# Performance work log

Hardware: AMD Instinct MI355X
Metric: run time of the kernel (lower is better)

The kernel has to match this reference:

```python
import jax, jax.numpy as jnp
import numpy as np


def _pdists(X):
    # Pairwise Euclidean distances (torch.cdist, p=2) via the Gram trick.
    sq = jnp.sum(X * X, axis=1)                      # (bs,)
    d2 = sq[:, None] + sq[None, :] - 2.0 * (X @ X.T)  # (bs, bs)
    d2 = jnp.maximum(d2, 0.0)
    # safe sqrt: exact forward, finite gradient at 0
    pos = d2 > 0
    return jnp.where(pos, jnp.sqrt(jnp.where(pos, d2, 1.0)), 0.0)


def setup_inputs() -> dict:
    key = jax.random.key(0)
    k1, k2, k3 = jax.random.split(key, 3)
    bs, d = 4096, 512
    n_classes, n_domains = 4, 3
    X = jax.random.normal(k1, (bs, d), dtype=jnp.float32)
    ds = jax.random.randint(k2, (bs,), 0, n_domains, dtype=jnp.int64 if jax.config.read('jax_enable_x64') else jnp.int32)
    y = jax.random.randint(k3, (bs,), 0, n_classes, dtype=jnp.int64 if jax.config.read('jax_enable_x64') else jnp.int32)
    return {"X": X, "ds": ds, "y": y, "n_classes": n_classes, "n_domains": n_domains}


def reference(X, ds, y, n_classes, n_domains):
    # Equivalent to JointCCSA.LSA / JointCCSA.LS with norm=True, assuming every
    # class and domain value appears in the batch (what torch.unique would find).
    dists = _pdists(X)                                # (bs, bs)

    d_lt = ds[:, None] < ds[None, :]                  # domain pair (d1 < d2) ordering
    same_y = y[:, None] == y[None, :]
    y_lt = y[:, None] < y[None, :]                    # class pair (c1 < c2) ordering

    # SA loss: 0.5 * sum over (i,j) with y_i==y_j, ds_i<ds_j
    sa_loss = 0.5 * jnp.sum(jnp.where(same_y & d_lt, dists, 0.0))
    n_sa = n_classes * (n_domains * (n_domains - 1) // 2)
    sa_loss = sa_loss / n_sa

    # S loss: hinge on margin=1, 0.5 * sum over (i,j) with y_i<y_j, ds_i<ds_j
    margin = 1.0
    h = jnp.maximum(0.0, margin - dists)
    s_loss = 0.5 * jnp.sum(jnp.where(y_lt & d_lt, h, 0.0))
    n_s = (n_classes * (n_classes - 1) // 2) * (n_domains * (n_domains - 1) // 2)
    s_loss = s_loss / n_s

    return sa_loss, s_loss
```

## Files before the change

### kernel.cpp

```cpp
#include <hip/hip_runtime.h>
#include <hip/hip_bf16.h>
#include <stdint.h>

#define NROW 4096
#define DIM  512
#define BM   128
#define BN   128
#define BK   64
#define NKT  (DIM / BK)

typedef __attribute__((ext_vector_type(8))) short  short8;
typedef __attribute__((ext_vector_type(4))) float  floatx4;

typedef const __attribute__((address_space(1))) void gvoid_t;
typedef __attribute__((address_space(3))) void       svoid_t;

__device__ __forceinline__ unsigned short f32_to_bf16_rne(float f) {
    unsigned u = __float_as_uint(f);
    u += 0x7FFFu + ((u >> 16) & 1u);
    return (unsigned short)(u >> 16);
}

__global__ __launch_bounds__(256) void prep_kernel(
    const float* __restrict__ X, unsigned short* __restrict__ Xb,
    float* __restrict__ sq, float* __restrict__ out)
{
    const int wave = threadIdx.x >> 6;
    const int lane = threadIdx.x & 63;
    const int row  = blockIdx.x * 4 + wave;
    const float4* xr = (const float4*)(X + (size_t)row * DIM);
    float4 v0 = xr[2 * lane];
    float4 v1 = xr[2 * lane + 1];
    float s = v0.x*v0.x + v0.y*v0.y + v0.z*v0.z + v0.w*v0.w
            + v1.x*v1.x + v1.y*v1.y + v1.z*v1.z + v1.w*v1.w;
    uint4 pk;
    pk.x = f32_to_bf16_rne(v0.x) | ((unsigned)f32_to_bf16_rne(v0.y) << 16);
    pk.y = f32_to_bf16_rne(v0.z) | ((unsigned)f32_to_bf16_rne(v0.w) << 16);
    pk.z = f32_to_bf16_rne(v1.x) | ((unsigned)f32_to_bf16_rne(v1.y) << 16);
    pk.w = f32_to_bf16_rne(v1.z) | ((unsigned)f32_to_bf16_rne(v1.w) << 16);
    *(uint4*)(Xb + (size_t)row * DIM + lane * 8) = pk;
    #pragma unroll
    for (int off = 32; off; off >>= 1) s += __shfl_xor(s, off);
    if (lane == 0) sq[row] = s;
    if (blockIdx.x == 0 && threadIdx.x < 2) out[threadIdx.x] = 0.0f;
}

__global__ __launch_bounds__(256) void ccsa_kernel(
    const unsigned short* __restrict__ Xb, const float* __restrict__ sq,
    const int* __restrict__ ds, const int* __restrict__ y,
    const int* __restrict__ ncls, const int* __restrict__ ndom,
    float* __restrict__ out)
{
    __shared__ __align__(16) unsigned short As[2][BM * BK];
    __shared__ __align__(16) unsigned short Bs[2][BN * BK];
    __shared__ float red[8];

    const int t = blockIdx.x;
    int r = (int)((sqrtf(8.0f * (float)t + 1.0f) - 1.0f) * 0.5f);
    while ((r + 1) * (r + 2) / 2 <= t) ++r;
    while (r * (r + 1) / 2 > t) --r;
    const int bj_t = r;
    const int bi_t = t - r * (r + 1) / 2;
    const bool diag = (bi_t == bj_t);
    const int bm0 = bi_t * BM;
    const int bn0 = bj_t * BN;

    const int tid    = threadIdx.x;
    const int wave   = tid >> 6;
    const int lane   = tid & 63;
    const int warp_m = wave >> 1;
    const int warp_n = wave & 1;

    floatx4 acc[4][4];
    #pragma unroll
    for (int a = 0; a < 4; ++a)
        #pragma unroll
        for (int b = 0; b < 4; ++b)
            acc[a][b] = (floatx4){0.f, 0.f, 0.f, 0.f};

    const int l3       = lane >> 3;
    const int c7       = lane & 7;
    const int srcchunk = c7 ^ l3;
    const int m15      = lane & 15;
    const int quad     = lane >> 4;
    const int row7     = lane & 7;

    #define STAGE(buf, kt)                                                    \
        do {                                                                  \
            const size_t kbase_ = (size_t)(kt) * BK + srcchunk * 8;           \
            _Pragma("unroll")                                                 \
            for (int is = 0; is < 4; ++is) {                                  \
                const int c  = is * 4 + wave;                                 \
                const int rA = bm0 + c * 8 + l3;                              \
                const int rB = bn0 + c * 8 + l3;                              \
                __builtin_amdgcn_global_load_lds(                             \
                    (gvoid_t*)(Xb + (size_t)rA * DIM + kbase_),               \
                    (svoid_t*)(&As[buf][c * 512]), 16, 0, 0);                 \
                __builtin_amdgcn_global_load_lds(                             \
                    (gvoid_t*)(Xb + (size_t)rB * DIM + kbase_),               \
                    (svoid_t*)(&Bs[buf][c * 512]), 16, 0, 0);                 \
            }                                                                 \
        } while (0)

    STAGE(0, 0);
    for (int kt = 0; kt < NKT; ++kt) {
        const int cur = kt & 1;
        __syncthreads();
        if (kt + 1 < NKT) STAGE(cur ^ 1, kt + 1);

        #pragma unroll
        for (int kh = 0; kh < 2; ++kh) {
            short8 a[4], b[4];
            #pragma unroll
            for (int tt = 0; tt < 4; ++tt) {
                const int rla   = warp_m * 64 + tt * 16 + m15;
                const int rlb   = warp_n * 64 + tt * 16 + m15;
                const int chunk = (kh * 4 + quad) ^ row7;
                a[tt] = *(const short8*)(&As[cur][rla * 64 + chunk * 8]);
                b[tt] = *(const short8*)(&Bs[cur][rlb * 64 + chunk * 8]);
            }
            #pragma unroll
            for (int tm = 0; tm < 4; ++tm)
                #pragma unroll
                for (int tn = 0; tn < 4; ++tn)
                    acc[tm][tn] = __builtin_amdgcn_mfma_f32_16x16x32_bf16(
                        a[tm], b[tn], acc[tm][tn], 0, 0, 0);
        }
    }
    #undef STAGE

    float sqj[4]; int yj[4], dsj[4];
    #pragma unroll
    for (int tn = 0; tn < 4; ++tn) {
        const int j = bn0 + warp_n * 64 + tn * 16 + m15;
        sqj[tn] = sq[j]; yj[tn] = y[j]; dsj[tn] = ds[j];
    }
    float sa = 0.f, ss = 0.f;
    if (diag) {
        #pragma unroll
        for (int tm = 0; tm < 4; ++tm) {
            #pragma unroll
            for (int rr = 0; rr < 4; ++rr) {
                const int i = bm0 + warp_m * 64 + tm * 16 + quad * 4 + rr;
                const float sqi = sq[i];
                const int   yi  = y[i];
                const int   dsi = ds[i];
                #pragma unroll
                for (int tn = 0; tn < 4; ++tn) {
                    if (dsi < dsj[tn]) {
                        const float d2   = sqi + sqj[tn] - 2.0f * acc[tm][tn][rr];
                        const float dist = sqrtf(fmaxf(d2, 0.f));
                        if (yi == yj[tn])     sa += dist;
                        else if (yi < yj[tn]) ss += fmaxf(0.f, 1.f - dist);
                    }
                }
            }
        }
    } else {
        #pragma unroll
        for (int tm = 0; tm < 4; ++tm) {
            #pragma unroll
            for (int rr = 0; rr < 4; ++rr) {
                const int i = bm0 + warp_m * 64 + tm * 16 + quad * 4 + rr;
                const float sqi = sq[i];
                const int   yi  = y[i];
                const int   dsi = ds[i];
                #pragma unroll
                for (int tn = 0; tn < 4; ++tn) {
                    if (dsi != dsj[tn]) {
                        const float d2   = sqi + sqj[tn] - 2.0f * acc[tm][tn][rr];
                        const float dist = sqrtf(fmaxf(d2, 0.f));
                        if (yi == yj[tn]) {
                            sa += dist;
                        } else {
                            const bool take = (dsi < dsj[tn]) ? (yi < yj[tn])
                                                              : (yj[tn] < yi);
                            if (take) ss += fmaxf(0.f, 1.f - dist);
                        }
                    }
                }
            }
        }
    }
    #pragma unroll
    for (int off = 32; off; off >>= 1) {
        sa += __shfl_xor(sa, off);
        ss += __shfl_xor(ss, off);
    }
    if (lane == 0) { red[wave] = sa; red[4 + wave] = ss; }
    __syncthreads();
    if (tid == 0) {
        const float tsa = red[0] + red[1] + red[2] + red[3];
        const float tss = red[4] + red[5] + red[6] + red[7];
        const int nc = *ncls, nd = *ndom;
        const float n_sa = (float)(nc * (nd * (nd - 1) / 2));
        const float n_s  = (float)((nc * (nc - 1) / 2) * (nd * (nd - 1) / 2));
        atomicAdd(out + 0, tsa * 0.5f / n_sa);
        atomicAdd(out + 1, tss * 0.5f / n_s);
    }
}

extern "C" void kernel_launch(void* const* d_in, const int* in_sizes, int n_in,
                              void* d_out, int out_size, void* d_ws, size_t ws_size,
                              hipStream_t stream) {
    (void)in_sizes; (void)n_in; (void)out_size; (void)ws_size;
    const float* X  = (const float*)d_in[0];
    const int*   ds = (const int*)d_in[1];
    const int*   y  = (const int*)d_in[2];
    const int*   nc = (const int*)d_in[3];
    const int*   nd = (const int*)d_in[4];
    float* out = (float*)d_out;

    unsigned short* Xb = (unsigned short*)d_ws;
    float* sq = (float*)((char*)d_ws + (size_t)NROW * DIM * 2);

    prep_kernel<<<NROW / 4, 256, 0, stream>>>(X, Xb, sq, out);
    const int ntiles = NROW / BM;
    const int nblocks = ntiles * (ntiles + 1) / 2;
    ccsa_kernel<<<nblocks, 256, 0, stream>>>(Xb, sq, ds, y, nc, nd, out);
}
```

Baseline: 107.8 us.

## Replace LDS-staged block GEMM with per-wave 64x64 register-pipelined tiles

Each wave now owns a 64x64 upper-triangular tile and loads bf16 operands straight from global memory into registers with a 4-stage software prefetch, dropping shared-memory staging and block barriers. The grid grows to cover four times as many smaller tiles to raise parallelism across CUs. This trades LDS reuse across waves for more global/L2 traffic and much higher register usage.

```diff
diff --git a/kernel.cpp b/kernel.cpp
--- a/kernel.cpp
+++ b/kernel.cpp
@@ -4,16 +4,12 @@
 
 #define NROW 4096
 #define DIM  512
-#define BM   128
-#define BN   128
-#define BK   64
-#define NKT  (DIM / BK)
+#define NT64 (NROW / 64)
+#define NTRI (NT64 * (NT64 + 1) / 2)
+#define NKS  (DIM / 32)
 
 typedef __attribute__((ext_vector_type(8))) short  short8;
 typedef __attribute__((ext_vector_type(4))) float  floatx4;
-
-typedef const __attribute__((address_space(1))) void gvoid_t;
-typedef __attribute__((address_space(3))) void       svoid_t;
 
 __device__ __forceinline__ unsigned short f32_to_bf16_rne(float f) {
     unsigned u = __float_as_uint(f);
@@ -45,31 +41,32 @@
     if (blockIdx.x == 0 && threadIdx.x < 2) out[threadIdx.x] = 0.0f;
 }
 
-__global__ __launch_bounds__(256) void ccsa_kernel(
+__global__ __launch_bounds__(256, 2) void ccsa_kernel(
     const unsigned short* __restrict__ Xb, const float* __restrict__ sq,
     const int* __restrict__ ds, const int* __restrict__ y,
     const int* __restrict__ ncls, const int* __restrict__ ndom,
     float* __restrict__ out)
 {
-    __shared__ __align__(16) unsigned short As[2][BM * BK];
-    __shared__ __align__(16) unsigned short Bs[2][BN * BK];
     __shared__ float red[8];
 
-    const int t = blockIdx.x;
-    int r = (int)((sqrtf(8.0f * (float)t + 1.0f) - 1.0f) * 0.5f);
-    while ((r + 1) * (r + 2) / 2 <= t) ++r;
-    while (r * (r + 1) / 2 > t) --r;
-    const int bj_t = r;
-    const int bi_t = t - r * (r + 1) / 2;
-    const bool diag = (bi_t == bj_t);
-    const int bm0 = bi_t * BM;
-    const int bn0 = bj_t * BN;
+    const int wave = threadIdx.x >> 6;
+    const int lane = threadIdx.x & 63;
+    const int g    = blockIdx.x * 4 + wave;
 
-    const int tid    = threadIdx.x;
-    const int wave   = tid >> 6;
-    const int lane   = tid & 63;
-    const int warp_m = wave >> 1;
-    const int warp_n = wave & 1;
+    int r = (int)((sqrtf(8.0f * (float)g + 1.0f) - 1.0f) * 0.5f);
+    while ((r + 1) * (r + 2) / 2 <= g) ++r;
+    while (r * (r + 1) / 2 > g) --r;
+    const int jt   = r;
+    const int it   = g - r * (r + 1) / 2;
+    const bool diag = (it == jt);
+    const int i0 = it * 64;
+    const int j0 = jt * 64;
+
+    const int m15  = lane & 15;
+    const int quad = lane >> 4;
+
+    const unsigned short* aptr = Xb + (size_t)(i0 + m15) * DIM + quad * 8;
+    const unsigned short* bptr = Xb + (size_t)(j0 + m15) * DIM + quad * 8;
 
     floatx4 acc[4][4];
     #pragma unroll
@@ -78,61 +75,37 @@
         for (int b = 0; b < 4; ++b)
             acc[a][b] = (floatx4){0.f, 0.f, 0.f, 0.f};
 
-    const int l3       = lane >> 3;
-    const int c7       = lane & 7;
-    const int srcchunk = c7 ^ l3;
-    const int m15      = lane & 15;
-    const int quad     = lane >> 4;
-    const int row7     = lane & 7;
+    short8 abuf[4][4], bbuf[4][4];
 
-    #define STAGE(buf, kt)                                                    \
+    #define LOADK(s, kt)                                                      \
         do {                                                                  \
-            const size_t kbase_ = (size_t)(kt) * BK + srcchunk * 8;           \
             _Pragma("unroll")                                                 \
-            for (int is = 0; is < 4; ++is) {                                  \
-                const int c  = is * 4 + wave;                                 \
-                const int rA = bm0 + c * 8 + l3;                              \
-                const int rB = bn0 + c * 8 + l3;                              \
-                __builtin_amdgcn_global_load_lds(                             \
-                    (gvoid_t*)(Xb + (size_t)rA * DIM + kbase_),               \
-                    (svoid_t*)(&As[buf][c * 512]), 16, 0, 0);                 \
-                __builtin_amdgcn_global_load_lds(                             \
-                    (gvoid_t*)(Xb + (size_t)rB * DIM + kbase_),               \
-                    (svoid_t*)(&Bs[buf][c * 512]), 16, 0, 0);                 \
+            for (int tt = 0; tt < 4; ++tt) {                                  \
+                abuf[s][tt] = *(const short8*)(aptr + tt * 16 * DIM + (kt) * 32); \
+                bbuf[s][tt] = *(const short8*)(bptr + tt * 16 * DIM + (kt) * 32); \
             }                                                                 \
         } while (0)
 
-    STAGE(0, 0);
-    for (int kt = 0; kt < NKT; ++kt) {
-        const int cur = kt & 1;
-        __syncthreads();
-        if (kt + 1 < NKT) STAGE(cur ^ 1, kt + 1);
-
+    LOADK(0, 0);
+    LOADK(1, 1);
+    LOADK(2, 2);
+    #pragma unroll
+    for (int kt = 0; kt < NKS; ++kt) {
+        const int s = kt & 3;
         #pragma unroll
-        for (int kh = 0; kh < 2; ++kh) {
-            short8 a[4], b[4];
+        for (int tm = 0; tm < 4; ++tm)
             #pragma unroll
-            for (int tt = 0; tt < 4; ++tt) {
-                const int rla   = warp_m * 64 + tt * 16 + m15;
-                const int rlb   = warp_n * 64 + tt * 16 + m15;
-                const int chunk = (kh * 4 + quad) ^ row7;
-                a[tt] = *(const short8*)(&As[cur][rla * 64 + chunk * 8]);
-                b[tt] = *(const short8*)(&Bs[cur][rlb * 64 + chunk * 8]);
-            }
-            #pragma unroll
-            for (int tm = 0; tm < 4; ++tm)
-                #pragma unroll
-                for (int tn = 0; tn < 4; ++tn)
-                    acc[tm][tn] = __builtin_amdgcn_mfma_f32_16x16x32_bf16(
-                        a[tm], b[tn], acc[tm][tn], 0, 0, 0);
-        }
+            for (int tn = 0; tn < 4; ++tn)
+                acc[tm][tn] = __builtin_amdgcn_mfma_f32_16x16x32_bf16(
+                    abuf[s][tm], bbuf[s][tn], acc[tm][tn], 0, 0, 0);
+        if (kt + 3 < NKS) LOADK((kt + 3) & 3, kt + 3);
     }
-    #undef STAGE
+    #undef LOADK
 
     float sqj[4]; int yj[4], dsj[4];
     #pragma unroll
     for (int tn = 0; tn < 4; ++tn) {
-        const int j = bn0 + warp_n * 64 + tn * 16 + m15;
+        const int j = j0 + tn * 16 + m15;
         sqj[tn] = sq[j]; yj[tn] = y[j]; dsj[tn] = ds[j];
     }
     float sa = 0.f, ss = 0.f;
@@ -141,7 +114,7 @@
         for (int tm = 0; tm < 4; ++tm) {
             #pragma unroll
             for (int rr = 0; rr < 4; ++rr) {
-                const int i = bm0 + warp_m * 64 + tm * 16 + quad * 4 + rr;
+                const int i = i0 + tm * 16 + quad * 4 + rr;
                 const float sqi = sq[i];
                 const int   yi  = y[i];
                 const int   dsi = ds[i];
@@ -161,7 +134,7 @@
         for (int tm = 0; tm < 4; ++tm) {
             #pragma unroll
             for (int rr = 0; rr < 4; ++rr) {
-                const int i = bm0 + warp_m * 64 + tm * 16 + quad * 4 + rr;
+                const int i = i0 + tm * 16 + quad * 4 + rr;
                 const float sqi = sq[i];
                 const int   yi  = y[i];
                 const int   dsi = ds[i];
@@ -189,7 +162,7 @@
     }
     if (lane == 0) { red[wave] = sa; red[4 + wave] = ss; }
     __syncthreads();
-    if (tid == 0) {
+    if (threadIdx.x == 0) {
         const float tsa = red[0] + red[1] + red[2] + red[3];
         const float tss = red[4] + red[5] + red[6] + red[7];
         const int nc = *ncls, nd = *ndom;
@@ -215,7 +188,5 @@
     float* sq = (float*)((char*)d_ws + (size_t)NROW * DIM * 2);
 
     prep_kernel<<<NROW / 4, 256, 0, stream>>>(X, Xb, sq, out);
-    const int ntiles = NROW / BM;
-    const int nblocks = ntiles * (ntiles + 1) / 2;
-    ccsa_kernel<<<nblocks, 256, 0, stream>>>(Xb, sq, ds, y, nc, nd, out);
+    ccsa_kernel<<<NTRI / 4, 256, 0, stream>>>(Xb, sq, ds, y, nc, nd, out);
 }
```

Measured after the change: 121.1 us. 1.12x slower.

## Pre-swizzle bf16 X into tile-contiguous layout and use 8 waves per block

Applied to the files above, without the earlier changes.

The prep kernel now writes bf16 X in a blocked layout where each 8-row group and k-tile forms a contiguous, pre-swizzled 1 KB chunk. Each global-to-LDS load is then a fully contiguous 1 KB read instead of 8 strided row segments. The GEMM block grows from 4 to 8 waves, each owning a 64x32 sub-tile, which halves per-wave accumulators and adds more waves per CU to hide latency. In exchange each wave issues more LDS A-fragment reads relative to its MFMA count, and the reduction now sums over 8 waves.

```diff
diff --git a/kernel.cpp b/kernel.cpp
--- a/kernel.cpp
+++ b/kernel.cpp
@@ -22,7 +22,7 @@
 }
 
 __global__ __launch_bounds__(256) void prep_kernel(
-    const float* __restrict__ X, unsigned short* __restrict__ Xb,
+    const float* __restrict__ X, unsigned short* __restrict__ Xpre,
     float* __restrict__ sq, float* __restrict__ out)
 {
     const int wave = threadIdx.x >> 6;
@@ -38,22 +38,26 @@
     pk.y = f32_to_bf16_rne(v0.z) | ((unsigned)f32_to_bf16_rne(v0.w) << 16);
     pk.z = f32_to_bf16_rne(v1.x) | ((unsigned)f32_to_bf16_rne(v1.y) << 16);
     pk.w = f32_to_bf16_rne(v1.z) | ((unsigned)f32_to_bf16_rne(v1.w) << 16);
-    *(uint4*)(Xb + (size_t)row * DIM + lane * 8) = pk;
+    const int G   = row >> 3;
+    const int l3r = row & 7;
+    const int kt  = lane >> 3;
+    const int p   = (lane & 7) ^ l3r;
+    *(uint4*)(Xpre + (size_t)G * 4096 + kt * 512 + l3r * 64 + p * 8) = pk;
     #pragma unroll
     for (int off = 32; off; off >>= 1) s += __shfl_xor(s, off);
     if (lane == 0) sq[row] = s;
     if (blockIdx.x == 0 && threadIdx.x < 2) out[threadIdx.x] = 0.0f;
 }
 
-__global__ __launch_bounds__(256) void ccsa_kernel(
-    const unsigned short* __restrict__ Xb, const float* __restrict__ sq,
+__global__ __launch_bounds__(512, 4) void ccsa_kernel(
+    const unsigned short* __restrict__ Xpre, const float* __restrict__ sq,
     const int* __restrict__ ds, const int* __restrict__ y,
     const int* __restrict__ ncls, const int* __restrict__ ndom,
     float* __restrict__ out)
 {
     __shared__ __align__(16) unsigned short As[2][BM * BK];
     __shared__ __align__(16) unsigned short Bs[2][BN * BK];
-    __shared__ float red[8];
+    __shared__ float red[16];
 
     const int t = blockIdx.x;
     int r = (int)((sqrtf(8.0f * (float)t + 1.0f) - 1.0f) * 0.5f);
@@ -64,41 +68,39 @@
     const bool diag = (bi_t == bj_t);
     const int bm0 = bi_t * BM;
     const int bn0 = bj_t * BN;
+    const int GA = bm0 >> 3;
+    const int GB = bn0 >> 3;
 
     const int tid    = threadIdx.x;
     const int wave   = tid >> 6;
     const int lane   = tid & 63;
-    const int warp_m = wave >> 1;
-    const int warp_n = wave & 1;
-
-    floatx4 acc[4][4];
+    const int warp_m = wave >> 2;
+    const int warp_n = wave & 3;
+
+    floatx4 acc[4][2];
     #pragma unroll
     for (int a = 0; a < 4; ++a)
         #pragma unroll
-        for (int b = 0; b < 4; ++b)
+        for (int b = 0; b < 2; ++b)
             acc[a][b] = (floatx4){0.f, 0.f, 0.f, 0.f};
 
-    const int l3       = lane >> 3;
-    const int c7       = lane & 7;
-    const int srcchunk = c7 ^ l3;
-    const int m15      = lane & 15;
-    const int quad     = lane >> 4;
-    const int row7     = lane & 7;
+    const int m15  = lane & 15;
+    const int quad = lane >> 4;
+    const int row7 = lane & 7;
 
     #define STAGE(buf, kt)                                                    \
         do {                                                                  \
-            const size_t kbase_ = (size_t)(kt) * BK + srcchunk * 8;           \
             _Pragma("unroll")                                                 \
-            for (int is = 0; is < 4; ++is) {                                  \
-                const int c  = is * 4 + wave;                                 \
-                const int rA = bm0 + c * 8 + l3;                              \
-                const int rB = bn0 + c * 8 + l3;                              \
+            for (int is = 0; is < 2; ++is) {                                  \
+                const int c = is * 8 + wave;                                  \
                 __builtin_amdgcn_global_load_lds(                             \
-                    (gvoid_t*)(Xb + (size_t)rA * DIM + kbase_),               \
-                    (svoid_t*)(&As[buf][c * 512]), 16, 0, 0);                 \
+                    (gvoid_t*)(Xpre + (size_t)(GA + c) * 4096 + (kt) * 512    \
+                               + lane * 8),                                   \
+                    (svoid_t*)(&As[buf][c * 512 + lane * 8]), 16, 0, 0);      \
                 __builtin_amdgcn_global_load_lds(                             \
-                    (gvoid_t*)(Xb + (size_t)rB * DIM + kbase_),               \
-                    (svoid_t*)(&Bs[buf][c * 512]), 16, 0, 0);                 \
+                    (gvoid_t*)(Xpre + (size_t)(GB + c) * 4096 + (kt) * 512    \
+                               + lane * 8),                                   \
+                    (svoid_t*)(&Bs[buf][c * 512 + lane * 8]), 16, 0, 0);      \
             }                                                                 \
         } while (0)
 
@@ -110,29 +112,32 @@
 
         #pragma unroll
         for (int kh = 0; kh < 2; ++kh) {
-            short8 a[4], b[4];
+            short8 a[4], b[2];
+            const int chunk = (kh * 4 + quad) ^ row7;
             #pragma unroll
             for (int tt = 0; tt < 4; ++tt) {
-                const int rla   = warp_m * 64 + tt * 16 + m15;
-                const int rlb   = warp_n * 64 + tt * 16 + m15;
-                const int chunk = (kh * 4 + quad) ^ row7;
+                const int rla = warp_m * 64 + tt * 16 + m15;
                 a[tt] = *(const short8*)(&As[cur][rla * 64 + chunk * 8]);
+            }
+            #pragma unroll
+            for (int tt = 0; tt < 2; ++tt) {
+                const int rlb = warp_n * 32 + tt * 16 + m15;
                 b[tt] = *(const short8*)(&Bs[cur][rlb * 64 + chunk * 8]);
             }
             #pragma unroll
             for (int tm = 0; tm < 4; ++tm)
                 #pragma unroll
-                for (int tn = 0; tn < 4; ++tn)
+                for (int tn = 0; tn < 2; ++tn)
                     acc[tm][tn] = __builtin_amdgcn_mfma_f32_16x16x32_bf16(
                         a[tm], b[tn], acc[tm][tn], 0, 0, 0);
         }
     }
     #undef STAGE
 
-    float sqj[4]; int yj[4], dsj[4];
-    #pragma unroll
-    for (int tn = 0; tn < 4; ++tn) {
-        const int j = bn0 + warp_n * 64 + tn * 16 + m15;
+    float sqj[2]; int yj[2], dsj[2];
+    #pragma unroll
+    for (int tn = 0; tn < 2; ++tn) {
+        const int j = bn0 + warp_n * 32 + tn * 16 + m15;
         sqj[tn] = sq[j]; yj[tn] = y[j]; dsj[tn] = ds[j];
     }
     float sa = 0.f, ss = 0.f;
@@ -146,7 +151,7 @@
                 const int   yi  = y[i];
                 const int   dsi = ds[i];
                 #pragma unroll
-                for (int tn = 0; tn < 4; ++tn) {
+                for (int tn = 0; tn < 2; ++tn) {
                     if (dsi < dsj[tn]) {
                         const float d2   = sqi + sqj[tn] - 2.0f * acc[tm][tn][rr];
                         const float dist = sqrtf(fmaxf(d2, 0.f));
@@ -166,7 +171,7 @@
                 const int   yi  = y[i];
                 const int   dsi = ds[i];
                 #pragma unroll
-                for (int tn = 0; tn < 4; ++tn) {
+                for (int tn = 0; tn < 2; ++tn) {
                     if (dsi != dsj[tn]) {
                         const float d2   = sqi + sqj[tn] - 2.0f * acc[tm][tn][rr];
                         const float dist = sqrtf(fmaxf(d2, 0.f));
@@ -187,11 +192,12 @@
         sa += __shfl_xor(sa, off);
         ss += __shfl_xor(ss, off);
     }
-    if (lane == 0) { red[wave] = sa; red[4 + wave] = ss; }
+    if (lane == 0) { red[wave] = sa; red[8 + wave] = ss; }
     __syncthreads();
     if (tid == 0) {
-        const float tsa = red[0] + red[1] + red[2] + red[3];
-        const float tss = red[4] + red[5] + red[6] + red[7];
+        float tsa = 0.f, tss = 0.f;
+        #pragma unroll
+        for (int w = 0; w < 8; ++w) { tsa += red[w]; tss += red[8 + w]; }
         const int nc = *ncls, nd = *ndom;
         const float n_sa = (float)(nc * (nd * (nd - 1) / 2));
         const float n_s  = (float)((nc * (nc - 1) / 2) * (nd * (nd - 1) / 2));
@@ -211,11 +217,11 @@
     const int*   nd = (const int*)d_in[4];
     float* out = (float*)d_out;
 
-    unsigned short* Xb = (unsigned short*)d_ws;
+    unsigned short* Xpre = (unsigned short*)d_ws;
     float* sq = (float*)((char*)d_ws + (size_t)NROW * DIM * 2);
 
-    prep_kernel<<<NROW / 4, 256, 0, stream>>>(X, Xb, sq, out);
+    prep_kernel<<<NROW / 4, 256, 0, stream>>>(X, Xpre, sq, out);
     const int ntiles = NROW / BM;
     const int nblocks = ntiles * (ntiles + 1) / 2;
-    ccsa_kernel<<<nblocks, 256, 0, stream>>>(Xb, sq, ds, y, nc, nd, out);
-}
+    ccsa_kernel<<<nblocks, 512, 0, stream>>>(Xpre, sq, ds, y, nc, nd, out);
+}
```

After: 98.90 us. -8.3%, faster.
